# Kernel tuning notes

Measured on AMD Instinct MI355X. Metric: run time of the kernel, lower is better.

Reference implementation:

```python
import jax, jax.numpy as jnp
import numpy as np
import math

N_QUBITS = 10
N_LAYERS = 2
HIDDEN = 768
VOCAB = 30522
DIM = 2 ** N_QUBITS


def _cnot_perm(c, t, n):
    # PennyLane convention: wire 0 is the most significant bit of the basis index.
    idx = np.arange(2 ** n)
    ctrl_bit = (idx >> (n - 1 - c)) & 1
    return jnp.asarray(idx ^ (ctrl_bit << (n - 1 - t)))

# BasicEntanglerLayers uses a CNOT ring: (0,1),(1,2),...,(n-1,0)
CNOT_PERMS = [_cnot_perm(q, (q + 1) % N_QUBITS, N_QUBITS) for q in range(N_QUBITS)]


def _apply_rx(state, theta, q):
    # state: (N, 2^n) complex, theta: (N,) per-sample RX angle on wire q.
    c = jnp.cos(theta * 0.5)[:, None, None]
    s = jnp.sin(theta * 0.5)[:, None, None]
    st = state.reshape(-1, 2 ** q, 2, DIM // (2 ** (q + 1)))
    a0, a1 = st[:, :, 0, :], st[:, :, 1, :]
    b0 = c * a0 - 1j * s * a1
    b1 = c * a1 - 1j * s * a0
    return jnp.stack([b0, b1], axis=2).reshape(state.shape)


def _quantum_probs(angles):
    # angles: (N, L, n). BasicEntanglerLayers = per-layer RX rotations + CNOT ring,
    # followed by qml.probs over all wires -> (N, 2^n).
    N = angles.shape[0]
    state = jnp.zeros((N, DIM), jnp.complex64).at[:, 0].set(1.0)
    for l in range(N_LAYERS):
        for q in range(N_QUBITS):
            state = _apply_rx(state, angles[:, l, q], q)
        for q in range(N_QUBITS):
            state = state[:, CNOT_PERMS[q]]
    return state.real ** 2 + state.imag ** 2


def _gelu(x):
    return x * 0.5 * (1.0 + jax.scipy.special.erf(x / math.sqrt(2.0)))


def setup_inputs() -> dict:
    key = jax.random.key(0)
    ks = jax.random.split(key, 4)
    B, S = 8, 512
    return {
        "hidden_states": jax.random.normal(ks[0], (B, S, HIDDEN), jnp.float32),
        "dense_w": jax.random.normal(ks[1], (HIDDEN, HIDDEN), jnp.float32) * 0.02,
        "dense_b": jnp.zeros((HIDDEN,), jnp.float32),
        "ln_w": jnp.ones((HIDDEN,), jnp.float32),
        "ln_b": jnp.zeros((HIDDEN,), jnp.float32),
        "ent_w": jax.random.normal(ks[2], (HIDDEN, N_LAYERS * N_QUBITS), jnp.float32) * 0.02,
        "ent_b": jnp.zeros((N_LAYERS * N_QUBITS,), jnp.float32),
        "proj_w": jax.random.normal(ks[3], (DIM, VOCAB), jnp.float32) * 0.02,
        "proj_b": jnp.zeros((VOCAB,), jnp.float32),
    }


def reference(hidden_states, dense_w, dense_b, ln_w, ln_b, ent_w, ent_b, proj_w, proj_b):
    # BertPredictionHeadTransform: dense -> gelu -> LayerNorm (eps inside sqrt)
    h = _gelu(hidden_states @ dense_w + dense_b)
    u = h.mean(-1, keepdims=True)
    v = ((h - u) ** 2).mean(-1, keepdims=True)
    h = ln_w * ((h - u) / jnp.sqrt(v + 1e-12)) + ln_b
    # entangle params -> sigmoid * 2pi, flatten batch to (N, L, n)
    ang = jax.nn.sigmoid(h @ ent_w + ent_b).reshape(-1, N_LAYERS, N_QUBITS) * (2.0 * math.pi)
    probs = _quantum_probs(ang)  # (B*S, 2^n)
    return probs @ proj_w + proj_b  # (B*S, vocab)
```

## Files before the change

kernel.cpp:

```cpp
#include <hip/hip_runtime.h>
#include <hip/hip_bf16.h>
#include <math.h>

#define HIDDEN 768
#define NROWS 4096
#define QDIM 1024
#define VOCAB 30522
#define NPAD 30592
#define NBX 239
#define NBY 32
#define NWG (NBX * NBY)

typedef _Float16 half8 __attribute__((ext_vector_type(8)));
typedef float floatx4 __attribute__((ext_vector_type(4)));

__device__ __forceinline__ void gload16(const _Float16* g, _Float16* l) {
  __builtin_amdgcn_global_load_lds(
      (const __attribute__((address_space(1))) void*)g,
      (__attribute__((address_space(3))) void*)l, 16, 0, 0);
}

__global__ __launch_bounds__(1024) void convert_transpose(
    const float* __restrict__ B, _Float16* __restrict__ BT) {
  __shared__ _Float16 tile[32][33];
  int n0 = blockIdx.x * 32;
  int k0 = blockIdx.y * 32;
  int tx = threadIdx.x, ty = threadIdx.y;
  int n = n0 + tx, k = k0 + ty;
  float v = (n < VOCAB) ? B[k * VOCAB + n] : 0.0f;
  tile[ty][tx] = (_Float16)v;
  __syncthreads();
  BT[(n0 + ty) * QDIM + (k0 + tx)] = tile[tx][ty];
}

__global__ __launch_bounds__(256) void gemm1_gelu(
    const float* __restrict__ A, const float* __restrict__ W,
    const float* __restrict__ bias, float* __restrict__ H) {
  __shared__ float As[64][17];
  __shared__ float Bs[16][68];
  int t = threadIdx.x;
  int bm = blockIdx.y * 64, bn = blockIdx.x * 64;
  int tx = t & 15, ty = t >> 4;
  float acc[4][4] = {};
  for (int k0 = 0; k0 < HIDDEN; k0 += 16) {
    {
      int r = t >> 2, c = (t & 3) * 4;
      float4 v = *(const float4*)&A[(bm + r) * HIDDEN + k0 + c];
      As[r][c] = v.x; As[r][c + 1] = v.y; As[r][c + 2] = v.z; As[r][c + 3] = v.w;
    }
    {
      int kr = t >> 4, c = (t & 15) * 4;
      float4 v = *(const float4*)&W[(k0 + kr) * HIDDEN + bn + c];
      Bs[kr][c] = v.x; Bs[kr][c + 1] = v.y; Bs[kr][c + 2] = v.z; Bs[kr][c + 3] = v.w;
    }
    __syncthreads();
#pragma unroll
    for (int k = 0; k < 16; k++) {
      float a[4], b[4];
#pragma unroll
      for (int i = 0; i < 4; i++) a[i] = As[ty * 4 + i][k];
#pragma unroll
      for (int j = 0; j < 4; j++) b[j] = Bs[k][tx * 4 + j];
#pragma unroll
      for (int i = 0; i < 4; i++)
#pragma unroll
        for (int j = 0; j < 4; j++) acc[i][j] += a[i] * b[j];
    }
    __syncthreads();
  }
#pragma unroll
  for (int i = 0; i < 4; i++) {
    int m = bm + ty * 4 + i;
#pragma unroll
    for (int j = 0; j < 4; j++) {
      int n = bn + tx * 4 + j;
      float x = acc[i][j] + bias[n];
      float g = x * 0.5f * (1.0f + erff(x * 0.70710678118654752f));
      H[m * HIDDEN + n] = g;
    }
  }
}

__device__ inline float block_sum256(float v, float* red) {
  int t = threadIdx.x;
#pragma unroll
  for (int o = 32; o > 0; o >>= 1) v += __shfl_down(v, o);
  __syncthreads();
  if ((t & 63) == 0) red[t >> 6] = v;
  __syncthreads();
  return red[0] + red[1] + red[2] + red[3];
}

__global__ __launch_bounds__(256) void row_quantum(
    const float* __restrict__ H, const float* __restrict__ ln_w,
    const float* __restrict__ ln_b, const float* __restrict__ ent_w,
    const float* __restrict__ ent_b, _Float16* __restrict__ probsA) {
  __shared__ float hn[HIDDEN];
  __shared__ float red[4];
  __shared__ float sr[QDIM];
  __shared__ float si[QDIM];
  __shared__ float ang[20];
  int t = threadIdx.x;
  int row = blockIdx.x;
  const float* hr = H + row * HIDDEN;

  float sum = 0.f;
  for (int i = t; i < HIDDEN; i += 256) {
    float v = hr[i];
    hn[i] = v;
    sum += v;
  }
  float u = block_sum256(sum, red) * (1.0f / HIDDEN);
  float vs = 0.f;
  for (int i = t; i < HIDDEN; i += 256) {
    float d = hn[i] - u;
    vs += d * d;
  }
  float var = block_sum256(vs, red) * (1.0f / HIDDEN);
  float inv = rsqrtf(var + 1e-12f);
  for (int i = t; i < HIDDEN; i += 256)
    hn[i] = ln_w[i] * ((hn[i] - u) * inv) + ln_b[i];
  __syncthreads();

  if (t < 20) {
    float acc = ent_b[t];
#pragma unroll 4
    for (int i = 0; i < HIDDEN; i++) acc += hn[i] * ent_w[i * 20 + t];
    float s = 1.0f / (1.0f + expf(-acc));
    ang[t] = 6.283185307179586f * s;
  }
  __syncthreads();

  for (int i = t; i < QDIM; i += 256) {
    sr[i] = (i == 0) ? 1.0f : 0.0f;
    si[i] = 0.0f;
  }
  __syncthreads();

  for (int l = 0; l < 2; l++) {
    for (int q = 0; q < 10; q++) {
      float th = ang[l * 10 + q] * 0.5f;
      float c = cosf(th), s = sinf(th);
      int bp = 9 - q;
      int mask = 1 << bp;
#pragma unroll
      for (int p = 0; p < 2; p++) {
        int pi = t + p * 256;
        int i0 = ((pi >> bp) << (bp + 1)) | (pi & (mask - 1));
        int i1 = i0 | mask;
        float a0r = sr[i0], a0i = si[i0], a1r = sr[i1], a1i = si[i1];
        sr[i0] = c * a0r + s * a1i;
        si[i0] = c * a0i - s * a1r;
        sr[i1] = c * a1r + s * a0i;
        si[i1] = c * a1i - s * a0r;
      }
      __syncthreads();
    }
    float tr[4], ti[4];
#pragma unroll
    for (int p = 0; p < 4; p++) {
      int i = t + p * 256;
      int j = i;
#pragma unroll
      for (int q = 9; q >= 0; q--) {
        int cb = 9 - q;
        int tb = 9 - ((q + 1) % 10);
        j ^= ((j >> cb) & 1) << tb;
      }
      tr[p] = sr[j];
      ti[p] = si[j];
    }
    __syncthreads();
#pragma unroll
    for (int p = 0; p < 4; p++) {
      int i = t + p * 256;
      sr[i] = tr[p];
      si[i] = ti[p];
    }
    __syncthreads();
  }

  for (int i = t; i < QDIM; i += 256) {
    float pv = sr[i] * sr[i] + si[i] * si[i];
    probsA[row * QDIM + i] = (_Float16)pv;
  }
}

__global__ __launch_bounds__(256) void gemm2_mfma(
    const _Float16* __restrict__ A,
    const _Float16* __restrict__ BT,
    const float* __restrict__ bias,
    float* __restrict__ C) {
  __shared__ _Float16 As[128][64];
  __shared__ _Float16 Bs[128][64];

  int t = threadIdx.x;
  int lane = t & 63, wave = t >> 6;
  int quad = lane >> 4, ln = lane & 15;
  int wm = (wave >> 1) * 64, wn = (wave & 1) * 64;

  int wg = blockIdx.x;
  int swz = (wg & 7) * (NWG / 8) + (wg >> 3);
  int bn = (swz >> 5) * 128;
  int bm = (swz & 31) * 128;

  int srow = t >> 3;
  int ps = t & 7;
  int lslot = ps ^ (srow & 7);
  const _Float16* gA = A  + (size_t)(bm + srow) * QDIM + lslot * 8;
  const _Float16* gB = BT + (size_t)(bn + srow) * QDIM + lslot * 8;
  _Float16* lA = &As[srow][ps * 8];
  _Float16* lB = &Bs[srow][ps * 8];

  int r7 = ln & 7;
  int off0 = ((0 * 4 + quad) ^ r7) * 8;
  int off1 = ((1 * 4 + quad) ^ r7) * 8;

  floatx4 acc[4][4];
#pragma unroll
  for (int i = 0; i < 4; i++)
#pragma unroll
    for (int j = 0; j < 4; j++) acc[i][j] = (floatx4){0.f, 0.f, 0.f, 0.f};

  for (int k0 = 0; k0 < QDIM; k0 += 64) {
#pragma unroll
    for (int i = 0; i < 4; i++) {
      gload16(gA + (size_t)i * 32 * QDIM + k0, lA + i * 32 * 64);
      gload16(gB + (size_t)i * 32 * QDIM + k0, lB + i * 32 * 64);
    }
    __syncthreads();
#pragma unroll
    for (int s = 0; s < 2; s++) {
      int off = s ? off1 : off0;
      half8 a[4], b[4];
#pragma unroll
      for (int i = 0; i < 4; i++) a[i] = *(const half8*)&As[wm + i * 16 + ln][off];
#pragma unroll
      for (int j = 0; j < 4; j++) b[j] = *(const half8*)&Bs[wn + j * 16 + ln][off];
#pragma unroll
      for (int i = 0; i < 4; i++)
#pragma unroll
        for (int j = 0; j < 4; j++)
          acc[i][j] = __builtin_amdgcn_mfma_f32_16x16x32_f16(a[i], b[j], acc[i][j], 0, 0, 0);
    }
    __syncthreads();
  }

#pragma unroll
  for (int j = 0; j < 4; j++) {
    int n = bn + wn + j * 16 + ln;
    if (n >= VOCAB) continue;
    float bv = bias[n];
#pragma unroll
    for (int i = 0; i < 4; i++) {
#pragma unroll
      for (int r = 0; r < 4; r++) {
        int m = bm + wm + i * 16 + quad * 4 + r;
        C[(size_t)m * VOCAB + n] = acc[i][j][r] + bv;
      }
    }
  }
}

extern "C" void kernel_launch(void* const* d_in, const int* in_sizes, int n_in,
                              void* d_out, int out_size, void* d_ws, size_t ws_size,
                              hipStream_t stream) {
  const float* hs      = (const float*)d_in[0];
  const float* dense_w = (const float*)d_in[1];
  const float* dense_b = (const float*)d_in[2];
  const float* ln_w    = (const float*)d_in[3];
  const float* ln_b    = (const float*)d_in[4];
  const float* ent_w   = (const float*)d_in[5];
  const float* ent_b   = (const float*)d_in[6];
  const float* proj_w  = (const float*)d_in[7];
  const float* proj_b  = (const float*)d_in[8];
  float* out = (float*)d_out;

  char* ws = (char*)d_ws;
  float*     h      = (float*)ws;
  _Float16*  probsA = (_Float16*)(ws + 12582912);
  _Float16*  BT     = (_Float16*)(ws + 20971520);

  hipLaunchKernelGGL(convert_transpose, dim3(NPAD / 32, QDIM / 32), dim3(32, 32), 0, stream,
                     proj_w, BT);
  hipLaunchKernelGGL(gemm1_gelu, dim3(HIDDEN / 64, NROWS / 64), dim3(256), 0, stream,
                     hs, dense_w, dense_b, h);
  hipLaunchKernelGGL(row_quantum, dim3(NROWS), dim3(256), 0, stream,
                     h, ln_w, ln_b, ent_w, ent_b, probsA);
  hipLaunchKernelGGL(gemm2_mfma, dim3(NWG), dim3(256), 0, stream,
                     probsA, BT, proj_b, out);
}
```

Measured before the change: 1.274 ms.

## Double-buffer LDS tiles in projection GEMM to overlap loads with MFMA

Converts the fp16 MFMA GEMM to a two-stage LDS ping-pong. The next K tile is issued via global_load_lds while the current tile is computed, with a partial vmcnt wait and raw barriers in place of __syncthreads. It also raises wave priority around the MFMA block. The aim is to hide global load latency behind compute, at the cost of doubling LDS per block (32KB), which may reduce occupancy. The hand-tuned waitcnt could risk races if the compiler reorders memory operations.

Result: no change. 1.281 ms (+0.5%).

```diff
diff --git a/kernel.cpp b/kernel.cpp
--- a/kernel.cpp
+++ b/kernel.cpp
@@ -10,6 +10,7 @@
 #define NBX 239
 #define NBY 32
 #define NWG (NBX * NBY)
+#define NT (QDIM / 64)
 
 typedef _Float16 half8 __attribute__((ext_vector_type(8)));
 typedef float floatx4 __attribute__((ext_vector_type(4)));
@@ -191,8 +192,8 @@
     const _Float16* __restrict__ BT,
     const float* __restrict__ bias,
     float* __restrict__ C) {
-  __shared__ _Float16 As[128][64];
-  __shared__ _Float16 Bs[128][64];
+  __shared__ _Float16 As[2][128][64];
+  __shared__ _Float16 Bs[2][128][64];
 
   int t = threadIdx.x;
   int lane = t & 63, wave = t >> 6;
@@ -209,8 +210,6 @@
   int lslot = ps ^ (srow & 7);
   const _Float16* gA = A  + (size_t)(bm + srow) * QDIM + lslot * 8;
   const _Float16* gB = BT + (size_t)(bn + srow) * QDIM + lslot * 8;
-  _Float16* lA = &As[srow][ps * 8];
-  _Float16* lB = &Bs[srow][ps * 8];
 
   int r7 = ln & 7;
   int off0 = ((0 * 4 + quad) ^ r7) * 8;
@@ -222,29 +221,46 @@
 #pragma unroll
     for (int j = 0; j < 4; j++) acc[i][j] = (floatx4){0.f, 0.f, 0.f, 0.f};
 
-  for (int k0 = 0; k0 < QDIM; k0 += 64) {
+  auto STAGE = [&](int kt, int b) {
 #pragma unroll
     for (int i = 0; i < 4; i++) {
-      gload16(gA + (size_t)i * 32 * QDIM + k0, lA + i * 32 * 64);
-      gload16(gB + (size_t)i * 32 * QDIM + k0, lB + i * 32 * 64);
-    }
-    __syncthreads();
+      gload16(gA + (size_t)i * 32 * QDIM + kt * 64, &As[b][srow + i * 32][ps * 8]);
+      gload16(gB + (size_t)i * 32 * QDIM + kt * 64, &Bs[b][srow + i * 32][ps * 8]);
+    }
+  };
+
+  auto COMPUTE = [&](int b) {
+    __builtin_amdgcn_s_setprio(1);
 #pragma unroll
     for (int s = 0; s < 2; s++) {
       int off = s ? off1 : off0;
-      half8 a[4], b[4];
-#pragma unroll
-      for (int i = 0; i < 4; i++) a[i] = *(const half8*)&As[wm + i * 16 + ln][off];
-#pragma unroll
-      for (int j = 0; j < 4; j++) b[j] = *(const half8*)&Bs[wn + j * 16 + ln][off];
+      half8 a[4], bb[4];
+#pragma unroll
+      for (int i = 0; i < 4; i++) a[i] = *(const half8*)&As[b][wm + i * 16 + ln][off];
+#pragma unroll
+      for (int j = 0; j < 4; j++) bb[j] = *(const half8*)&Bs[b][wn + j * 16 + ln][off];
 #pragma unroll
       for (int i = 0; i < 4; i++)
 #pragma unroll
         for (int j = 0; j < 4; j++)
-          acc[i][j] = __builtin_amdgcn_mfma_f32_16x16x32_f16(a[i], b[j], acc[i][j], 0, 0, 0);
-    }
-    __syncthreads();
-  }
+          acc[i][j] = __builtin_amdgcn_mfma_f32_16x16x32_f16(a[i], bb[j], acc[i][j], 0, 0, 0);
+    }
+    __builtin_amdgcn_s_setprio(0);
+  };
+
+  STAGE(0, 0);
+  int cur = 0;
+  for (int kt = 0; kt < NT - 1; ++kt) {
+    STAGE(kt + 1, cur ^ 1);
+    asm volatile("s_waitcnt vmcnt(8)" ::: "memory");
+    __builtin_amdgcn_s_barrier();
+    COMPUTE(cur);
+    __builtin_amdgcn_s_barrier();
+    cur ^= 1;
+  }
+  asm volatile("s_waitcnt vmcnt(0)" ::: "memory");
+  __builtin_amdgcn_s_barrier();
+  COMPUTE(cur);
 
 #pragma unroll
   for (int j = 0; j < 4; j++) {
```
